# Performance work log

Hardware: AMD Instinct MI355X
Metric: run time of the kernel (lower is better)

The kernel has to match this reference:

```python
import jax, jax.numpy as jnp
import numpy as np
from jax import lax

B = 256
INPUT_DIM = 65536
SEQ = 128
VOCAB = INPUT_DIM // SEQ  # 512
LATENT = 128
HIDS = (1024, 512, 256)   # encoder hidden dims (hidden_dims[:-1])
ENC_OUT = 128             # hidden_dims[-1]
GRU_H = 128               # decoder hidden_dim = hidden_dims[-1]
BN_EPS = 1e-5
LRELU_SLOPE = 0.01


def setup_inputs() -> dict:
    key = jax.random.key(0)
    ks = iter(jax.random.split(key, 40))
    def w(shape, scale=0.02):
        return (jax.random.normal(next(ks), shape, dtype=jnp.float32) * scale)
    d = {}
    d['x'] = jax.random.normal(next(ks), (B, INPUT_DIM), dtype=jnp.float32)
    d['eps'] = jax.random.normal(next(ks), (B, LATENT), dtype=jnp.float32)
    dims = (INPUT_DIM,) + HIDS
    # encoder Linear+BN stacks
    for i in range(3):
        d[f'W{i}'] = w((dims[i + 1], dims[i]))
        d[f'b{i}'] = w((dims[i + 1],))
        d[f'g{i}'] = jnp.ones((dims[i + 1],), jnp.float32)
        d[f'be{i}'] = jnp.zeros((dims[i + 1],), jnp.float32)
    d['Wout'] = w((ENC_OUT, HIDS[-1]))
    d['bout'] = w((ENC_OUT,))
    d['Wmu'] = w((LATENT, ENC_OUT)); d['bmu'] = w((LATENT,))
    d['Wlv'] = w((LATENT, ENC_OUT)); d['blv'] = w((LATENT,))
    # GRU (num_layers=1), PyTorch gate order r,z,n
    d['Wih'] = w((3 * GRU_H, LATENT)); d['bih'] = w((3 * GRU_H,))
    d['Whh'] = w((3 * GRU_H, GRU_H)); d['bhh'] = w((3 * GRU_H,))
    d['Wfc'] = w((VOCAB, GRU_H)); d['bfc'] = w((VOCAB,))
    return d


def _bn(h, g, b):
    m = jnp.mean(h, axis=0)
    v = jnp.var(h, axis=0)
    return (h - m) * lax.rsqrt(v + BN_EPS) * g + b


def _lrelu(h):
    return jnp.where(h > 0, h, LRELU_SLOPE * h)


def reference(x, eps, W0, b0, g0, be0, W1, b1, g1, be1, W2, b2, g2, be2,
              Wout, bout, Wmu, bmu, Wlv, blv, Wih, bih, Whh, bhh, Wfc, bfc):
    # ---- encode ----
    h = x
    for W, b, g, be in ((W0, b0, g0, be0), (W1, b1, g1, be1), (W2, b2, g2, be2)):
        h = _lrelu(_bn(h @ W.T + b, g, be))
    h = h @ Wout.T + bout
    h1 = jax.nn.relu(h)
    mu = h1 @ Wmu.T + bmu
    logvar = h1 @ Wlv.T + blv
    # ---- reparameterize ----
    z = mu + eps * jnp.exp(0.5 * logvar)
    # ---- greedy decode: GRU step + argmax + one-hot, seq_length times ----
    # GRU input is the constant z each step -> precompute input projection once
    xp = z @ Wih.T + bih                       # [B, 3H]
    xr, xz, xn = jnp.split(xp, 3, axis=1)
    h0 = jnp.zeros((x.shape[0], GRU_H), x.dtype)

    def step(hid, _):
        hp = hid @ Whh.T + bhh
        hr, hz, hn = jnp.split(hp, 3, axis=1)
        r = jax.nn.sigmoid(xr + hr)
        zg = jax.nn.sigmoid(xz + hz)
        n = jnp.tanh(xn + r * hn)
        h2 = (1.0 - zg) * n + zg * hid
        logits = h2 @ Wfc.T + bfc              # [B, V]
        oh = jax.nn.one_hot(jnp.argmax(logits, axis=1), VOCAB, dtype=logits.dtype)
        return h2, oh

    _, outs = lax.scan(step, h0, None, length=SEQ)  # [S, B, V]
    out = jnp.transpose(outs, (1, 0, 2))            # [B, S, V]
    return out, mu, logvar
```

## Files before the change

kernel.cpp:

```cpp
#include <hip/hip_runtime.h>

#define DI __device__ __forceinline__

typedef __attribute__((ext_vector_type(8))) short s16x8;
typedef __attribute__((ext_vector_type(4))) float f32x4;

DI f32x4 mfma16(s16x8 a, s16x8 b, f32x4 c) {
  return __builtin_amdgcn_mfma_f32_16x16x32_bf16(a, b, c, 0, 0, 0);
}

DI unsigned short f2bf(float f) {
  unsigned int u = __builtin_bit_cast(unsigned int, f);
  u += 0x7fffu + ((u >> 16) & 1u);
  return (unsigned short)(u >> 16);
}
DI float bf2f(unsigned short h) {
  unsigned int u = ((unsigned int)h) << 16;
  return __builtin_bit_cast(float, u);
}
DI void split2(float f, unsigned short &hi, unsigned short &lo) {
  hi = f2bf(f);
  lo = f2bf(f - bf2f(hi));
}
DI void write_pair4(unsigned short* hp, unsigned short* lp, float4 v) {
  unsigned short h0,h1,h2,h3,l0,l1,l2,l3;
  split2(v.x,h0,l0); split2(v.y,h1,l1); split2(v.z,h2,l2); split2(v.w,h3,l3);
  *(ushort4*)hp = make_ushort4(h0,h1,h2,h3);
  *(ushort4*)lp = make_ushort4(l0,l1,l2,l3);
}

template<int M, int N, int K, int KS, bool SWZ>
__global__ __launch_bounds__(256, 2) void k_gemm(const float* __restrict__ A,
                                                 const float* __restrict__ Bw,
                                                 float* __restrict__ P) {
  constexpr int MT = M / 128, NT = N / 128;
  constexpr int KC = K / KS;
  constexpr int ITERS = KC / 32;
  int bid = blockIdx.x;
  int kidx, mt, nt;
  if (SWZ) {
    int xcd = bid & 7, s = bid >> 3;
    kidx = xcd + 8 * (s >> 4);
    int mn = s & 15; mt = mn >> 3; nt = mn & 7;
  } else {
    kidx = bid / (MT * NT);
    int mn = bid % (MT * NT);
    mt = mn / NT; nt = mn % NT;
  }
  int tid = threadIdx.x;
  int w = tid >> 6, lane = tid & 63, q = lane >> 4, l15 = lane & 15;
  int wm = w >> 1, wn = w & 1;

  __shared__ unsigned short Ah[2][4][128][8], Al[2][4][128][8];
  __shared__ unsigned short Bh[2][4][128][8], Bl[2][4][128][8];

  int srow = tid >> 1;
  int skb  = (tid & 1) * 16;
  const float* Abase = A  + (size_t)(mt * 128 + srow) * K + (size_t)kidx * KC;
  const float* Bbase = Bw + (size_t)(nt * 128 + srow) * K + (size_t)kidx * KC;

  float4 ra[4], rb[4];
  auto loadit = [&](int it) {
    const float* pa = Abase + it * 32 + skb;
    const float* pb = Bbase + it * 32 + skb;
#pragma unroll
    for (int i = 0; i < 4; i++) {
      ra[i] = *(const float4*)(pa + 4 * i);
      rb[i] = *(const float4*)(pb + 4 * i);
    }
  };
  auto stage = [&](int pb) {
#pragma unroll
    for (int i = 0; i < 4; i++) {
      int k0 = skb + 4 * i, qq = k0 >> 3, j0 = k0 & 7;
      write_pair4(&Ah[pb][qq][srow][j0], &Al[pb][qq][srow][j0], ra[i]);
      write_pair4(&Bh[pb][qq][srow][j0], &Bl[pb][qq][srow][j0], rb[i]);
    }
  };

  f32x4 acc[4][4];
#pragma unroll
  for (int i = 0; i < 4; i++)
#pragma unroll
    for (int j = 0; j < 4; j++) acc[i][j] = (f32x4){0.f, 0.f, 0.f, 0.f};

  loadit(0);
  stage(0);
  loadit(1);

  for (int it = 0; it < ITERS; ++it) {
    __syncthreads();
    if (it + 1 < ITERS) stage((it + 1) & 1);
    if (it + 2 < ITERS) loadit(it + 2);
    int pr = it & 1;

    s16x8 afh[4], afl[4], bfh[4], bfl[4];
#pragma unroll
    for (int t = 0; t < 4; t++) {
      int m = wm * 64 + 16 * t + l15;
      afh[t] = *(const s16x8*)&Ah[pr][q][m][0];
      afl[t] = *(const s16x8*)&Al[pr][q][m][0];
      int n = wn * 64 + 16 * t + l15;
      bfh[t] = *(const s16x8*)&Bh[pr][q][n][0];
      bfl[t] = *(const s16x8*)&Bl[pr][q][n][0];
    }
#pragma unroll
    for (int ti = 0; ti < 4; ti++)
#pragma unroll
      for (int tj = 0; tj < 4; tj++) {
        acc[ti][tj] = mfma16(afh[ti], bfh[tj], acc[ti][tj]);
        acc[ti][tj] = mfma16(afl[ti], bfh[tj], acc[ti][tj]);
        acc[ti][tj] = mfma16(afh[ti], bfl[tj], acc[ti][tj]);
      }
  }
#pragma unroll
  for (int ti = 0; ti < 4; ti++)
#pragma unroll
    for (int tj = 0; tj < 4; tj++)
#pragma unroll
      for (int r = 0; r < 4; r++) {
        int row = mt * 128 + wm * 64 + 16 * ti + 4 * q + r;
        int col = nt * 128 + wn * 64 + 16 * tj + l15;
        P[((size_t)kidx * M + row) * N + col] = acc[ti][tj][r];
      }
}

template<int KS>
__global__ __launch_bounds__(256) void k_red(const float* __restrict__ P,
                                             float* __restrict__ O) {
  int idx = blockIdx.x * 256 + threadIdx.x;
  float s = 0.f;
#pragma unroll
  for (int kk = 0; kk < KS; kk++) s += P[(size_t)kk * 262144 + idx];
  O[idx] = s;
}

template<int KS, int N>
__global__ __launch_bounds__(256) void k_bn(const float* __restrict__ P,
                                            const float* __restrict__ g,
                                            const float* __restrict__ be,
                                            float* __restrict__ a) {
  int tid = threadIdx.x;
  int c = tid & 15, bg = tid >> 4;
  int col = blockIdx.x * 16 + c;
  __shared__ float hbuf[256][16];
  __shared__ float sbuf[16][16], s2buf[16][16];
  __shared__ float msc[16], msh[16];
  float s = 0.f, s2 = 0.f;
  for (int b = bg * 16; b < bg * 16 + 16; b++) {
    float h = 0.f;
#pragma unroll
    for (int kk = 0; kk < KS; kk++) h += P[((size_t)kk * 256 + b) * N + col];
    hbuf[b][c] = h;
    s += h; s2 += h * h;
  }
  sbuf[bg][c] = s; s2buf[bg][c] = s2;
  __syncthreads();
  if (bg == 0) {
    float ts = 0.f, ts2 = 0.f;
#pragma unroll
    for (int i = 0; i < 16; i++) { ts += sbuf[i][c]; ts2 += s2buf[i][c]; }
    float m = ts * (1.f / 256.f);
    float v = ts2 * (1.f / 256.f) - m * m;
    float rs = rsqrtf(v + 1e-5f);
    float sc = g[col] * rs;
    msc[c] = sc;
    msh[c] = be[col] - m * sc;
  }
  __syncthreads();
  float sc = msc[c], sh = msh[c];
  for (int b = bg * 16; b < bg * 16 + 16; b++) {
    float v = hbuf[b][c] * sc + sh;
    a[(size_t)b * N + col] = v > 0.f ? v : 0.01f * v;
  }
}

__global__ __launch_bounds__(128) void k_head(const float* __restrict__ P3,
    const float* __restrict__ bout,
    const float* __restrict__ Wmu, const float* __restrict__ bmu,
    const float* __restrict__ Wlv, const float* __restrict__ blv,
    const float* __restrict__ Wih, const float* __restrict__ bih,
    const float* __restrict__ eps,
    float* __restrict__ out_mu, float* __restrict__ out_lv,
    float* __restrict__ xp) {
  int b = blockIdx.x, j = threadIdx.x;
  __shared__ float es[128], zs[128];
  float e = P3[(size_t)b * 128 + j] + P3[(size_t)(256 + b) * 128 + j] + bout[j];
  es[j] = e > 0.f ? e : 0.f;
  __syncthreads();
  float mu = bmu[j], lv = blv[j];
  for (int k = 0; k < 128; k++) {
    mu += es[k] * Wmu[j * 128 + k];
    lv += es[k] * Wlv[j * 128 + k];
  }
  out_mu[b * 128 + j] = mu;
  out_lv[b * 128 + j] = lv;
  float z = mu + eps[b * 128 + j] * expf(0.5f * lv);
  zs[j] = z;
  __syncthreads();
  for (int gi = 0; gi < 3; gi++) {
    int row = gi * 128 + j;
    float s = bih[row];
    for (int k = 0; k < 128; k++) s += zs[k] * Wih[row * 128 + k];
    xp[(size_t)b * 384 + row] = s;
  }
}

__global__ __launch_bounds__(256, 1) void k_gru(const float* __restrict__ Whh,
    const float* __restrict__ bhh, const float* __restrict__ xp,
    float* __restrict__ H) {
  int b0 = blockIdx.x * 16;
  int tid = threadIdx.x;
  int w = tid >> 6, lane = tid & 63, q = lane >> 4, l15 = lane & 15;
  __shared__ unsigned short h2hi[2][16][136], h2lo[2][16][136];
  __shared__ float hbuf[2][16][132];
  (void)lane;

  int rb6[6];
  rb6[0] = 32 * w;        rb6[1] = 32 * w + 16;
  rb6[2] = 128 + 32 * w;  rb6[3] = 128 + 32 * w + 16;
  rb6[4] = 256 + 32 * w;  rb6[5] = 256 + 32 * w + 16;

  s16x8 wfh[6][4], wfl[6][4];
#pragma unroll
  for (int t = 0; t < 6; t++)
#pragma unroll
    for (int kt = 0; kt < 4; kt++) {
      const float* p = Whh + (size_t)(rb6[t] + l15) * 128 + kt * 32 + q * 8;
      s16x8 hi, lo;
#pragma unroll
      for (int j = 0; j < 8; j++) {
        unsigned short h, l; split2(p[j], h, l);
        hi[j] = (short)h; lo[j] = (short)l;
      }
      wfh[t][kt] = hi; wfl[t][kt] = lo;
    }

  int gb = b0 + l15;
  float xr_[2][4], xz_[2][4], xn_[2][4], bhn_[2][4], hprev[2][4];
#pragma unroll
  for (int t = 0; t < 2; t++)
#pragma unroll
    for (int r = 0; r < 4; r++) {
      int k0 = 32 * w + 16 * t + 4 * q + r;
      xr_[t][r] = xp[(size_t)gb * 384 + k0] + bhh[k0];
      xz_[t][r] = xp[(size_t)gb * 384 + 128 + k0] + bhh[128 + k0];
      xn_[t][r] = xp[(size_t)gb * 384 + 256 + k0];
      bhn_[t][r] = bhh[256 + k0];
      hprev[t][r] = 0.f;
    }

  for (int i = tid; i < 16 * 136; i += 256) {
    (&h2hi[0][0][0])[i] = 0;
    (&h2lo[0][0][0])[i] = 0;
  }
  __syncthreads();

  int hrow = tid >> 4, hcol = (tid & 15) * 8;

  for (int s = 0; s < 128; s++) {
    int p = s & 1;
    s16x8 bhf[4], blf[4];
#pragma unroll
    for (int kt = 0; kt < 4; kt++) {
      bhf[kt] = *(const s16x8*)&h2hi[p][l15][kt * 32 + q * 8];
      blf[kt] = *(const s16x8*)&h2lo[p][l15][kt * 32 + q * 8];
    }
    if (s > 0) {
      float4 v0 = *(const float4*)&hbuf[p ^ 1][hrow][hcol];
      float4 v1 = *(const float4*)&hbuf[p ^ 1][hrow][hcol + 4];
      float* dst = H + ((size_t)(b0 + hrow) * 128 + (s - 1)) * 128 + hcol;
      *(float4*)dst = v0;
      *(float4*)(dst + 4) = v1;
    }

    f32x4 acc[6];
#pragma unroll
    for (int t = 0; t < 6; t++) acc[t] = (f32x4){0.f, 0.f, 0.f, 0.f};
#pragma unroll
    for (int t = 0; t < 6; t++)
#pragma unroll
      for (int kt = 0; kt < 4; kt++) {
        acc[t] = mfma16(wfh[t][kt], bhf[kt], acc[t]);
        acc[t] = mfma16(wfl[t][kt], bhf[kt], acc[t]);
        acc[t] = mfma16(wfh[t][kt], blf[kt], acc[t]);
      }

#pragma unroll
    for (int t = 0; t < 2; t++) {
      unsigned short hs[4], ls[4];
      float hv[4];
#pragma unroll
      for (int r = 0; r < 4; r++) {
        float hr = acc[t][r], hz = acc[2 + t][r], hn = acc[4 + t][r];
        float rg = 1.f / (1.f + expf(-(xr_[t][r] + hr)));
        float zg = 1.f / (1.f + expf(-(xz_[t][r] + hz)));
        float ng = tanhf(xn_[t][r] + rg * (hn + bhn_[t][r]));
        float h2 = zg * (hprev[t][r] - ng) + ng;
        hprev[t][r] = h2;
        hv[r] = h2;
        split2(h2, hs[r], ls[r]);
      }
      int kb = 32 * w + 16 * t + 4 * q;
      *(float4*)&hbuf[p][l15][kb] = make_float4(hv[0], hv[1], hv[2], hv[3]);
      *(ushort4*)&h2hi[p ^ 1][l15][kb] = make_ushort4(hs[0], hs[1], hs[2], hs[3]);
      *(ushort4*)&h2lo[p ^ 1][l15][kb] = make_ushort4(ls[0], ls[1], ls[2], ls[3]);
    }
    __syncthreads();
  }
  {
    float4 v0 = *(const float4*)&hbuf[1][hrow][hcol];
    float4 v1 = *(const float4*)&hbuf[1][hrow][hcol + 4];
    float* dst = H + ((size_t)(b0 + hrow) * 128 + 127) * 128 + hcol;
    *(float4*)dst = v0;
    *(float4*)(dst + 4) = v1;
  }
}

__global__ __launch_bounds__(256, 2) void k_fc(const float* __restrict__ H,
    const float* __restrict__ Wfc, const float* __restrict__ bfc,
    float* __restrict__ out) {
  int rows0 = blockIdx.x * 64;
  int tid = threadIdx.x;
  int w = tid >> 6, lane = tid & 63, q = lane >> 4, l15 = lane & 15;
  __shared__ unsigned short Ah[4][4][64][8], Al[4][4][64][8];
  __shared__ unsigned short Bh[4][4][32][8], Bl[4][4][32][8];
  __shared__ int argbuf[64];
  (void)lane;

  {
    int row = tid >> 2, kb = (tid & 3) * 32;
    const float* p = H + (size_t)(rows0 + row) * 128 + kb;
#pragma unroll
    for (int i = 0; i < 8; i++) {
      float4 v = *(const float4*)(p + 4 * i);
      int k0 = kb + 4 * i;
      int kt = k0 >> 5, qq = (k0 >> 3) & 3, j0 = k0 & 7;
      write_pair4(&Ah[kt][qq][row][j0], &Al[kt][qq][row][j0], v);
    }
  }
  __syncthreads();

  s16x8 afh[4], afl[4];
#pragma unroll
  for (int kt = 0; kt < 4; kt++) {
    afh[kt] = *(const s16x8*)&Ah[kt][q][16 * w + l15][0];
    afl[kt] = *(const s16x8*)&Al[kt][q][16 * w + l15][0];
  }

  float best[4]; int bidx[4];
#pragma unroll
  for (int r = 0; r < 4; r++) { best[r] = -3.4e38f; bidx[r] = 0; }

  for (int c = 0; c < 16; c++) {
    {
      int n = tid >> 3, kb = (tid & 7) * 16;
      const float* p = Wfc + (size_t)(c * 32 + n) * 128 + kb;
#pragma unroll
      for (int i = 0; i < 4; i++) {
        float4 v = *(const float4*)(p + 4 * i);
        int k0 = kb + 4 * i;
        int kt = k0 >> 5, qq = (k0 >> 3) & 3, j0 = k0 & 7;
        write_pair4(&Bh[kt][qq][n][j0], &Bl[kt][qq][n][j0], v);
      }
    }
    __syncthreads();
    f32x4 acc[2];
    acc[0] = (f32x4){0.f, 0.f, 0.f, 0.f};
    acc[1] = (f32x4){0.f, 0.f, 0.f, 0.f};
#pragma unroll
    for (int nt = 0; nt < 2; nt++)
#pragma unroll
      for (int kt = 0; kt < 4; kt++) {
        s16x8 bh = *(const s16x8*)&Bh[kt][q][nt * 16 + l15][0];
        s16x8 bl = *(const s16x8*)&Bl[kt][q][nt * 16 + l15][0];
        acc[nt] = mfma16(afh[kt], bh, acc[nt]);
        acc[nt] = mfma16(afl[kt], bh, acc[nt]);
        acc[nt] = mfma16(afh[kt], bl, acc[nt]);
      }
#pragma unroll
    for (int nt = 0; nt < 2; nt++)
#pragma unroll
      for (int r = 0; r < 4; r++) {
        int col = c * 32 + nt * 16 + l15;
        float v = acc[nt][r] + bfc[col];
        if (v > best[r]) { best[r] = v; bidx[r] = col; }
      }
    __syncthreads();
  }

#pragma unroll
  for (int r = 0; r < 4; r++) {
    float bv = best[r]; int bi = bidx[r];
    for (int off = 8; off >= 1; off >>= 1) {
      float ov = __shfl_xor(bv, off, 64);
      int oi = __shfl_xor(bi, off, 64);
      if (ov > bv || (ov == bv && oi < bi)) { bv = ov; bi = oi; }
    }
    if (l15 == 0) argbuf[16 * w + 4 * q + r] = bi;
  }
  __syncthreads();

  int row = tid >> 2, cb = (tid & 3) * 128;
  int am = argbuf[row];
  float* op = out + (size_t)(rows0 + row) * 512 + cb;
#pragma unroll
  for (int i = 0; i < 32; i++) {
    float4 v = {0.f, 0.f, 0.f, 0.f};
    int base = cb + 4 * i;
    if (am >= base && am < base + 4) ((float*)&v)[am - base] = 1.0f;
    *(float4*)(op + 4 * i) = v;
  }
}

extern "C" void kernel_launch(void* const* d_in, const int* in_sizes, int n_in,
                              void* d_out, int out_size, void* d_ws, size_t ws_size,
                              hipStream_t stream) {
  const float* x    = (const float*)d_in[0];
  const float* eps  = (const float*)d_in[1];
  const float* W0   = (const float*)d_in[2];
  const float* g0   = (const float*)d_in[4];
  const float* be0  = (const float*)d_in[5];
  const float* W1   = (const float*)d_in[6];
  const float* g1   = (const float*)d_in[8];
  const float* be1  = (const float*)d_in[9];
  const float* W2   = (const float*)d_in[10];
  const float* g2   = (const float*)d_in[12];
  const float* be2  = (const float*)d_in[13];
  const float* Wout = (const float*)d_in[14];
  const float* bout = (const float*)d_in[15];
  const float* Wmu  = (const float*)d_in[16];
  const float* bmu  = (const float*)d_in[17];
  const float* Wlv  = (const float*)d_in[18];
  const float* blv  = (const float*)d_in[19];
  const float* Wih  = (const float*)d_in[20];
  const float* bih  = (const float*)d_in[21];
  const float* Whh  = (const float*)d_in[22];
  const float* bhh  = (const float*)d_in[23];
  const float* Wfc  = (const float*)d_in[24];
  const float* bfc  = (const float*)d_in[25];

  float* out    = (float*)d_out;
  float* mu_out = out + 16777216;
  float* lv_out = out + 16777216 + 32768;

  const bool big = ws_size >= 75900000ull;
  const int KS0 = big ? 64 : 16;

  float* ws  = (float*)d_ws;
  float* P0  = ws;
  float* O0  = ws + (size_t)262144 * KS0;
  float* a1  = O0 + 262144;
  float* P1  = a1 + 262144;
  float* a2  = P1 + 1048576;
  float* P2  = a2 + 131072;
  float* a3  = P2 + 262144;
  float* P3  = a3 + 65536;
  float* xp  = P3 + 65536;
  float* Hst = ws;

  if (big) {
    hipLaunchKernelGGL((k_gemm<256,1024,65536,64,true>), dim3(1024), dim3(256), 0, stream, x, W0, P0);
    hipLaunchKernelGGL((k_red<64>),                      dim3(1024), dim3(256), 0, stream, P0, O0);
  } else {
    hipLaunchKernelGGL((k_gemm<256,1024,65536,16,true>), dim3(256),  dim3(256), 0, stream, x, W0, P0);
    hipLaunchKernelGGL((k_red<16>),                      dim3(1024), dim3(256), 0, stream, P0, O0);
  }
  hipLaunchKernelGGL((k_bn<1,1024>),                   dim3(64),  dim3(256), 0, stream, O0, g0, be0, a1);
  hipLaunchKernelGGL((k_gemm<256,512,1024,8,false>),   dim3(64),  dim3(256), 0, stream, a1, W1, P1);
  hipLaunchKernelGGL((k_bn<8,512>),                    dim3(32),  dim3(256), 0, stream, P1, g1, be1, a2);
  hipLaunchKernelGGL((k_gemm<256,256,512,4,false>),    dim3(16),  dim3(256), 0, stream, a2, W2, P2);
  hipLaunchKernelGGL((k_bn<4,256>),                    dim3(16),  dim3(256), 0, stream, P2, g2, be2, a3);
  hipLaunchKernelGGL((k_gemm<256,128,256,2,false>),    dim3(4),   dim3(256), 0, stream, a3, Wout, P3);
  hipLaunchKernelGGL(k_head, dim3(256), dim3(128), 0, stream, P3, bout, Wmu, bmu, Wlv, blv, Wih, bih, eps, mu_out, lv_out, xp);
  hipLaunchKernelGGL(k_gru,  dim3(16),  dim3(256), 0, stream, Whh, bhh, xp, Hst);
  hipLaunchKernelGGL(k_fc,   dim3(512), dim3(256), 0, stream, Hst, Wfc, bfc, out);
}
```

Before: 975.0 us.

## Batch GRU hidden-state stores, split MFMA accumulators, use fast gate math

The GRU recurrence kernel now keeps the last nine hidden states in a shared-memory ring buffer and writes them to global memory eight steps at a time, instead of storing one step per iteration. The three bf16-split MFMA products are accumulated into two independent accumulator sets in an interleaved gate order, shortening the dependency chains inside each step. Sigmoid and tanh switch to fast exp plus hardware reciprocal. The trade-off is extra LDS and slightly reduced precision in the gate nonlinearities.

```diff
diff --git a/kernel.cpp b/kernel.cpp
--- a/kernel.cpp
+++ b/kernel.cpp
@@ -28,6 +28,9 @@
   *(ushort4*)hp = make_ushort4(h0,h1,h2,h3);
   *(ushort4*)lp = make_ushort4(l0,l1,l2,l3);
 }
+
+DI float fsig(float x)  { return __builtin_amdgcn_rcpf(1.f + __expf(-x)); }
+DI float ftanhf(float x){ return 1.f - 2.f * __builtin_amdgcn_rcpf(1.f + __expf(2.f * x)); }
 
 template<int M, int N, int K, int KS, bool SWZ>
 __global__ __launch_bounds__(256, 2) void k_gemm(const float* __restrict__ A,
@@ -213,7 +216,7 @@
   int tid = threadIdx.x;
   int w = tid >> 6, lane = tid & 63, q = lane >> 4, l15 = lane & 15;
   __shared__ unsigned short h2hi[2][16][136], h2lo[2][16][136];
-  __shared__ float hbuf[2][16][132];
+  __shared__ float hstage[9][16][132];
   (void)lane;
 
   int rb6[6];
@@ -257,6 +260,7 @@
   __syncthreads();
 
   int hrow = tid >> 4, hcol = (tid & 15) * 8;
+  int sl = 0;
 
   for (int s = 0; s < 128; s++) {
     int p = s & 1;
@@ -266,25 +270,37 @@
       bhf[kt] = *(const s16x8*)&h2hi[p][l15][kt * 32 + q * 8];
       blf[kt] = *(const s16x8*)&h2lo[p][l15][kt * 32 + q * 8];
     }
-    if (s > 0) {
-      float4 v0 = *(const float4*)&hbuf[p ^ 1][hrow][hcol];
-      float4 v1 = *(const float4*)&hbuf[p ^ 1][hrow][hcol + 4];
-      float* dst = H + ((size_t)(b0 + hrow) * 128 + (s - 1)) * 128 + hcol;
-      *(float4*)dst = v0;
-      *(float4*)(dst + 4) = v1;
-    }
-
-    f32x4 acc[6];
-#pragma unroll
-    for (int t = 0; t < 6; t++) acc[t] = (f32x4){0.f, 0.f, 0.f, 0.f};
-#pragma unroll
-    for (int t = 0; t < 6; t++)
+    if ((s & 7) == 0 && s) {
+      int fb = s - 8;
+#pragma unroll
+      for (int ss = 0; ss < 8; ss++) {
+        int t9 = sl + 1 + ss;
+        int fsl = t9 >= 9 ? t9 - 9 : t9;
+        float4 v0 = *(const float4*)&hstage[fsl][hrow][hcol];
+        float4 v1 = *(const float4*)&hstage[fsl][hrow][hcol + 4];
+        float* dst = H + ((size_t)(b0 + hrow) * 128 + fb + ss) * 128 + hcol;
+        *(float4*)dst = v0;
+        *(float4*)(dst + 4) = v1;
+      }
+    }
+
+    f32x4 accm[6], accc[6];
+#pragma unroll
+    for (int t = 0; t < 6; t++) {
+      accm[t] = (f32x4){0.f, 0.f, 0.f, 0.f};
+      accc[t] = (f32x4){0.f, 0.f, 0.f, 0.f};
+    }
+    const int ord[6] = {0, 2, 4, 1, 3, 5};
+#pragma unroll
+    for (int oi = 0; oi < 6; oi++) {
+      int t = ord[oi];
 #pragma unroll
       for (int kt = 0; kt < 4; kt++) {
-        acc[t] = mfma16(wfh[t][kt], bhf[kt], acc[t]);
-        acc[t] = mfma16(wfl[t][kt], bhf[kt], acc[t]);
-        acc[t] = mfma16(wfh[t][kt], blf[kt], acc[t]);
-      }
+        accm[t] = mfma16(wfh[t][kt], bhf[kt], accm[t]);
+        accc[t] = mfma16(wfl[t][kt], bhf[kt], accc[t]);
+        accc[t] = mfma16(wfh[t][kt], blf[kt], accc[t]);
+      }
+    }
 
 #pragma unroll
     for (int t = 0; t < 2; t++) {
@@ -292,26 +308,32 @@
       float hv[4];
 #pragma unroll
       for (int r = 0; r < 4; r++) {
-        float hr = acc[t][r], hz = acc[2 + t][r], hn = acc[4 + t][r];
-        float rg = 1.f / (1.f + expf(-(xr_[t][r] + hr)));
-        float zg = 1.f / (1.f + expf(-(xz_[t][r] + hz)));
-        float ng = tanhf(xn_[t][r] + rg * (hn + bhn_[t][r]));
-        float h2 = zg * (hprev[t][r] - ng) + ng;
+        float hr = accm[t][r] + accc[t][r];
+        float hz = accm[2 + t][r] + accc[2 + t][r];
+        float hn = accm[4 + t][r] + accc[4 + t][r];
+        float rg = fsig(xr_[t][r] + hr);
+        float zg = fsig(xz_[t][r] + hz);
+        float ng = ftanhf(fmaf(rg, hn + bhn_[t][r], xn_[t][r]));
+        float h2 = fmaf(zg, hprev[t][r] - ng, ng);
         hprev[t][r] = h2;
         hv[r] = h2;
         split2(h2, hs[r], ls[r]);
       }
       int kb = 32 * w + 16 * t + 4 * q;
-      *(float4*)&hbuf[p][l15][kb] = make_float4(hv[0], hv[1], hv[2], hv[3]);
+      *(float4*)&hstage[sl][l15][kb] = make_float4(hv[0], hv[1], hv[2], hv[3]);
       *(ushort4*)&h2hi[p ^ 1][l15][kb] = make_ushort4(hs[0], hs[1], hs[2], hs[3]);
       *(ushort4*)&h2lo[p ^ 1][l15][kb] = make_ushort4(ls[0], ls[1], ls[2], ls[3]);
     }
+    sl = (sl == 8) ? 0 : sl + 1;
     __syncthreads();
   }
-  {
-    float4 v0 = *(const float4*)&hbuf[1][hrow][hcol];
-    float4 v1 = *(const float4*)&hbuf[1][hrow][hcol + 4];
-    float* dst = H + ((size_t)(b0 + hrow) * 128 + 127) * 128 + hcol;
+#pragma unroll
+  for (int ss = 0; ss < 8; ss++) {
+    int fb = 120 + ss;
+    int fsl = fb % 9;
+    float4 v0 = *(const float4*)&hstage[fsl][hrow][hcol];
+    float4 v1 = *(const float4*)&hstage[fsl][hrow][hcol + 4];
+    float* dst = H + ((size_t)(b0 + hrow) * 128 + fb) * 128 + hcol;
     *(float4*)dst = v0;
     *(float4*)(dst + 4) = v1;
   }
```

After: 865.6 us. -11.2%, faster.
